# Kernel optimization log

Measured on AMD Instinct MI355X. Metric: run time of the kernel, lower is better.

Reference implementation:

```python
import jax, jax.numpy as jnp
import numpy as np

B, S, H, NH, HD = 2, 2048, 2048, 16, 128


def _bit_linear(x, w):
    """Ternary STE BitLinear: absmean scaling, round/clamp, fp matmul, rescale."""
    eps = 1e-5
    wn = w / (jnp.abs(w).mean() + eps)
    # straight-through estimator: forward uses quantized weights, grad flows to wn
    wq = wn + jax.lax.stop_gradient(jnp.clip(jnp.round(wn), -1.0, 1.0) - wn)
    y = x @ wq.T
    scale = w.shape[1]  # in_features
    Qb = 128.0  # 2**(8-1)
    return jnp.clip(y / scale * Qb, -Qb, Qb)


def _rotate_half(x):
    x1, x2 = jnp.split(x, 2, axis=-1)
    return jnp.concatenate([-x2, x1], axis=-1)


def setup_inputs() -> dict:
    key = jax.random.key(0)
    k1, k2, k3 = jax.random.split(key, 3)
    x = jax.random.normal(k1, (B, S, H), dtype=jnp.float32)
    w_qkv = jax.random.normal(k2, (3 * H, H), dtype=jnp.float32) * 0.02
    w_o = jax.random.normal(k3, (H, H), dtype=jnp.float32) * 0.02
    # realistic RoPE table [2, S, HD]
    inv_freq = 1.0 / (10000.0 ** (jnp.arange(0, HD, 2, dtype=jnp.float32) / HD))
    freqs = jnp.arange(S, dtype=jnp.float32)[:, None] * inv_freq[None, :]
    emb = jnp.concatenate([freqs, freqs], axis=-1)  # [S, HD]
    rotary = jnp.stack([jnp.cos(emb), jnp.sin(emb)], axis=0)
    return {"x": x, "rotary": rotary, "w_qkv": w_qkv, "w_o": w_o}


def reference(x, rotary, w_qkv, w_o):
    qkv = _bit_linear(x, w_qkv)  # [B, S, 3H]
    q, k, v = jnp.split(qkv, 3, axis=-1)
    q = q.reshape(B, S, NH, HD)
    k = k.reshape(B, S, NH, HD)
    v = v.reshape(B, S, NH, HD)
    cos = rotary[0][None, :, None, :]  # [1, S, 1, HD]
    sin = rotary[1][None, :, None, :]
    q = q * cos + _rotate_half(q) * sin
    k = k * cos + _rotate_half(k) * sin
    # [B, NH, S, HD]
    q, k, v = (t.transpose(0, 2, 1, 3) for t in (q, k, v))
    scores = jnp.einsum("bhqd,bhkd->bhqk", q, k) / np.sqrt(HD).astype(np.float32)
    causal = jnp.tril(jnp.ones((S, S), dtype=bool))
    scores = jnp.where(causal[None, None], scores, -jnp.inf)
    attn = jax.nn.softmax(scores, axis=-1)
    y = jnp.einsum("bhqk,bhkd->bhqd", attn, v)
    y = y.transpose(0, 2, 1, 3).reshape(B, S, H)
    return _bit_linear(y, w_o)
```

## Files before the change

### kernel.cpp

```cpp
#include <hip/hip_runtime.h>
#include <hip/hip_bf16.h>
#include <stdint.h>

#define B_   2
#define S_   2048
#define H_   2048
#define NH_  16
#define HD_  128
#define MTOK 4096
#define NQKV 6144

typedef unsigned short u16;
typedef __attribute__((ext_vector_type(8))) __bf16 bf16x8;
typedef __attribute__((ext_vector_type(4))) float f32x4;
typedef __attribute__((ext_vector_type(16))) float f32x16;

static __device__ __forceinline__ float bf2f(u16 u){
  union { uint32_t i; float f; } v; v.i = ((uint32_t)u) << 16; return v.f;
}
static __device__ __forceinline__ u16 f2bf(float f){
  union { float f; uint32_t i; } v; v.f = f;
  uint32_t r = v.i + 0x7FFFu + ((v.i >> 16) & 1u);
  return (u16)(r >> 16);
}
static __device__ __forceinline__ uint32_t cvt_pk_bf16(float lo, float hi){
  uint32_t r;
  asm("v_cvt_pk_bf16_f32 %0, %1, %2" : "=v"(r) : "v"(lo), "v"(hi));
  return r;
}
static __device__ __forceinline__ void pl32swap(uint32_t &a, uint32_t &b){
  asm volatile("v_permlane32_swap_b32 %0, %1" : "+v"(a), "+v"(b));
}

__device__ __forceinline__ void gload_lds16(const void* g, void* l){
  __builtin_amdgcn_global_load_lds((const __attribute__((address_space(1))) void*)g,
                                   (__attribute__((address_space(3))) void*)l, 16, 0, 0);
}

__global__ void absum_kernel(const float* __restrict__ w, int n, float* __restrict__ partial){
  __shared__ float sm[256];
  float s = 0.f;
  for (int i = blockIdx.x*256 + threadIdx.x; i < n; i += gridDim.x*256)
    s += fabsf(w[i]);
  sm[threadIdx.x] = s; __syncthreads();
  for (int st = 128; st > 0; st >>= 1){
    if ((int)threadIdx.x < st) sm[threadIdx.x] += sm[threadIdx.x + st];
    __syncthreads();
  }
  if (threadIdx.x == 0) partial[blockIdx.x] = sm[0];
}

__global__ void finalize_kernel(const float* __restrict__ p1, const float* __restrict__ p2,
                                float* __restrict__ scales){
  __shared__ double sm[256];
  int t = threadIdx.x;
  double s = (double)p1[t] + (double)p1[t+256] + (double)p1[t+512] + (double)p1[t+768];
  sm[t] = s; __syncthreads();
  for (int st = 128; st > 0; st >>= 1){ if (t < st) sm[t] += sm[t+st]; __syncthreads(); }
  if (t == 0) scales[0] = (float)(1.0 / (sm[0] / (double)(3*H_*H_) + 1e-5));
  __syncthreads();
  s = (double)p2[t] + (double)p2[t+256] + (double)p2[t+512] + (double)p2[t+768];
  sm[t] = s; __syncthreads();
  for (int st = 128; st > 0; st >>= 1){ if (t < st) sm[t] += sm[t+st]; __syncthreads(); }
  if (t == 0) scales[1] = (float)(1.0 / (sm[0] / (double)(H_*H_) + 1e-5));
}

__global__ void quant_kernel(const float* __restrict__ w, u16* __restrict__ wq, int n,
                             const float* __restrict__ scales, int which){
  float inv = scales[which];
  for (int i = blockIdx.x*256 + threadIdx.x; i < n; i += gridDim.x*256){
    float q = rintf(w[i] * inv);
    q = fminf(1.f, fmaxf(-1.f, q));
    wq[i] = f2bf(q);
  }
}

__global__ void castx_kernel(const float* __restrict__ x, u16* __restrict__ xb, int n){
  int i = blockIdx.x*256 + threadIdx.x;
  if (i < n) xb[i] = f2bf(x[i]);
}

template<int EPI>
__global__ __launch_bounds__(256, 4) void gemm_kernel(const u16* __restrict__ A,
    const u16* __restrict__ Bw, int M, int N, int K,
    float* __restrict__ outf, u16* __restrict__ qb, u16* __restrict__ kb, u16* __restrict__ vtb)
{
  __shared__ u16 As[128*32];
  __shared__ u16 Bs[128*32];
  int nbn = N >> 7;
  int nb_tot = (M >> 7) * nbn;
  int bid = blockIdx.x;
  int chunk = nb_tot >> 3;
  bid = (bid & 7) * chunk + (bid >> 3);
  int bm = bid / nbn, bn = bid % nbn;
  int m0 = bm << 7, n0 = bn << 7;
  int tid = threadIdx.x;
  int lane = tid & 63, wid = tid >> 6;
  int wr = wid >> 1, wc = wid & 1;
  int lg = lane >> 4, lr = lane & 15;

  const u16* Ab = A + m0 * K;
  const u16* Bb = Bw + n0 * K;
  int srow = tid >> 2;
  int scol = (tid & 3) << 3;

  f32x4 acc[4][4];
  #pragma unroll
  for (int i = 0; i < 4; i++)
    #pragma unroll
    for (int j = 0; j < 4; j++) acc[i][j] = f32x4{0.f,0.f,0.f,0.f};

  for (int k0 = 0; k0 < K; k0 += 32){
    gload_lds16(Ab + srow*K      + k0 + scol, As + tid*8);
    gload_lds16(Ab + (srow+64)*K + k0 + scol, As + 2048 + tid*8);
    gload_lds16(Bb + srow*K      + k0 + scol, Bs + tid*8);
    gload_lds16(Bb + (srow+64)*K + k0 + scol, Bs + 2048 + tid*8);
    __syncthreads();
    bf16x8 af[4], bfr[4];
    #pragma unroll
    for (int mi = 0; mi < 4; mi++) af[mi]  = *(const bf16x8*)(As + ((wr*64 + mi*16 + lr)*32 + lg*8));
    #pragma unroll
    for (int ni = 0; ni < 4; ni++) bfr[ni] = *(const bf16x8*)(Bs + ((wc*64 + ni*16 + lr)*32 + lg*8));
    #pragma unroll
    for (int mi = 0; mi < 4; mi++)
      #pragma unroll
      for (int ni = 0; ni < 4; ni++)
        acc[mi][ni] = __builtin_amdgcn_mfma_f32_16x16x32_bf16(af[mi], bfr[ni], acc[mi][ni], 0, 0, 0);
    __syncthreads();
  }

  #pragma unroll
  for (int mi = 0; mi < 4; mi++){
    #pragma unroll
    for (int ni = 0; ni < 4; ni++){
      int ncol = n0 + wc*64 + ni*16 + lr;
      #pragma unroll
      for (int r = 0; r < 4; r++){
        int m = m0 + wr*64 + mi*16 + lg*4 + r;
        float v = acc[mi][ni][r] * 0.0625f;
        v = fminf(128.f, fmaxf(-128.f, v));
        if (EPI == 1){
          outf[m*N + ncol] = v;
        } else {
          int b = m >> 11, s = m & 2047;
          int part = ncol >> 11, c = ncol & 2047;
          int h = c >> 7, d = c & 127;
          int bh = b*NH_ + h;
          u16 bv = f2bf(v);
          if (part == 0)      qb[((bh*S_ + s) << 7) + d] = bv;
          else if (part == 1) kb[((bh*S_ + s) << 7) + d] = bv;
          else                vtb[((bh*HD_ + d) << 11) + s] = bv;
        }
      }
    }
  }
}

__global__ void rope_kernel(u16* __restrict__ qb, u16* __restrict__ kb, const float* __restrict__ rot){
  int i = blockIdx.x*256 + threadIdx.x;
  int d = i & 63;
  int s = (i >> 6) & 2047;
  int bh = (i >> 17) & 31;
  u16* buf = (i >> 22) ? kb : qb;
  int base = (bh*S_ + s)*HD_;
  float c  = rot[s*HD_ + d];
  float sn = rot[S_*HD_ + s*HD_ + d];
  float x1 = bf2f(buf[base + d]);
  float x2 = bf2f(buf[base + d + 64]);
  buf[base + d]      = f2bf(x1*c - x2*sn);
  buf[base + d + 64] = f2bf(x2*c + x1*sn);
}

__global__ __launch_bounds__(256) void attn_kernel(const u16* __restrict__ qb,
    const u16* __restrict__ kb, const u16* __restrict__ vtb, u16* __restrict__ ao)
{
  __shared__ alignas(16) u16 Ks[2][4096];
  __shared__ alignas(16) u16 Vs[2][4096];

  int bid = blockIdx.x;
  int sbid = (bid & 7)*64 + (bid >> 3);
  int bh = sbid >> 4;
  int bq = 15 - (sbid & 15);
  int tid = threadIdx.x;
  int wid = tid >> 6, lane = tid & 63;
  int l31 = lane & 31, hl = lane >> 5;
  int q0 = bq * 128;
  int qw = q0 + wid*32;
  int q  = qw + l31;

  const u16* Qp = qb + (size_t)(bh*S_ + qw)*HD_;
  const u16* Kp = kb + (size_t)bh*S_*HD_;
  const u16* Vt = vtb + (size_t)bh*HD_*S_;

  bf16x8 qf[8];
  #pragma unroll
  for (int t = 0; t < 8; t++)
    qf[t] = *(const bf16x8*)(Qp + l31*HD_ + t*16 + hl*8);

  f32x16 o[4];
  #pragma unroll
  for (int i = 0; i < 4; i++)
    #pragma unroll
    for (int j = 0; j < 16; j++) o[i][j] = 0.f;
  float m_r = -1e30f, l_r = 0.f;
  const float sm_scale = 0.08838834764831845f;

  auto STAGE = [&](int buf, int kt2){
    int t0 = wid*2;
    gload_lds16(Kp + (size_t)(kt2 + l31)*HD_ + (t0  )*16 + hl*8, &Ks[buf][((t0  )*64 + lane)*8]);
    gload_lds16(Kp + (size_t)(kt2 + l31)*HD_ + (t0+1)*16 + hl*8, &Ks[buf][((t0+1)*64 + lane)*8]);
    int v0 = wid*2, v1 = wid*2 + 1;
    gload_lds16(Vt + (size_t)((v0&3)*32 + l31)*S_ + kt2 + (v0>>2)*16 + hl*8, &Vs[buf][(v0*64 + lane)*8]);
    gload_lds16(Vt + (size_t)((v1&3)*32 + l31)*S_ + kt2 + (v1>>2)*16 + hl*8, &Vs[buf][(v1*64 + lane)*8]);
  };

  int n_it = 4*bq + 4;
  STAGE(0, 0);
  int cur = 0, kt = 0;
  for (int it = 0; it < n_it; ++it, kt += 32){
    if (it + 1 < n_it){
      STAGE(cur ^ 1, kt + 32);
      asm volatile("s_waitcnt vmcnt(4)" ::: "memory");
    } else {
      asm volatile("s_waitcnt vmcnt(0)" ::: "memory");
    }
    __builtin_amdgcn_sched_barrier(0);
    __builtin_amdgcn_s_barrier();

    if (kt <= qw){
      f32x16 sa;
      #pragma unroll
      for (int j = 0; j < 16; j++) sa[j] = 0.f;
      #pragma unroll
      for (int t = 0; t < 8; t++){
        bf16x8 kf = *(const bf16x8*)(&Ks[cur][(t*64 + lane)*8]);
        sa = __builtin_amdgcn_mfma_f32_32x32x16_bf16(kf, qf[t], sa, 0, 0, 0);
      }

      float sv[16];
      if (kt == qw){
        #pragma unroll
        for (int r = 0; r < 16; r++){
          int key = kt + (r&3) + 8*(r>>2) + 4*hl;
          sv[r] = (key > q) ? -1e30f : sa[r]*sm_scale;
        }
      } else {
        #pragma unroll
        for (int r = 0; r < 16; r++) sv[r] = sa[r]*sm_scale;
      }

      float pm = sv[0];
      #pragma unroll
      for (int r = 1; r < 16; r++) pm = fmaxf(pm, sv[r]);
      pm = fmaxf(pm, __shfl_xor(pm, 32));
      if (!__all(pm - m_r <= 8.f)){
        float mn = fmaxf(m_r, pm);
        float scl = __expf(m_r - mn);
        m_r = mn; l_r *= scl;
        #pragma unroll
        for (int i = 0; i < 4; i++)
          #pragma unroll
          for (int j = 0; j < 16; j++) o[i][j] *= scl;
      }
      float p[16];
      #pragma unroll
      for (int r = 0; r < 16; r++) p[r] = __expf(sv[r] - m_r);
      float ts = 0.f;
      #pragma unroll
      for (int r = 0; r < 16; r++) ts += p[r];
      ts += __shfl_xor(ts, 32);
      l_r += ts;

      uint32_t a0 = cvt_pk_bf16(p[0],  p[1]),  a1 = cvt_pk_bf16(p[2],  p[3]);
      uint32_t a2 = cvt_pk_bf16(p[4],  p[5]),  a3 = cvt_pk_bf16(p[6],  p[7]);
      uint32_t b0 = cvt_pk_bf16(p[8],  p[9]),  b1 = cvt_pk_bf16(p[10], p[11]);
      uint32_t b2 = cvt_pk_bf16(p[12], p[13]), b3 = cvt_pk_bf16(p[14], p[15]);
      pl32swap(a0, a2); pl32swap(a1, a3);
      pl32swap(b0, b2); pl32swap(b1, b3);
      union { uint32_t u[4]; bf16x8 v; } pf0, pf1;
      pf0.u[0]=a0; pf0.u[1]=a1; pf0.u[2]=a2; pf0.u[3]=a3;
      pf1.u[0]=b0; pf1.u[1]=b1; pf1.u[2]=b2; pf1.u[3]=b3;

      #pragma unroll
      for (int db = 0; db < 4; db++){
        bf16x8 vf0 = *(const bf16x8*)(&Vs[cur][((0*4 + db)*64 + lane)*8]);
        o[db] = __builtin_amdgcn_mfma_f32_32x32x16_bf16(vf0, pf0.v, o[db], 0, 0, 0);
        bf16x8 vf1 = *(const bf16x8*)(&Vs[cur][((1*4 + db)*64 + lane)*8]);
        o[db] = __builtin_amdgcn_mfma_f32_32x32x16_bf16(vf1, pf1.v, o[db], 0, 0, 0);
      }
      asm volatile("s_waitcnt lgkmcnt(0)" ::: "memory");
    }
    __builtin_amdgcn_sched_barrier(0);
    __builtin_amdgcn_s_barrier();
    cur ^= 1;
  }

  float inv = 1.f / l_r;
  int b = bh >> 4, hh = bh & 15;
  u16* orow = ao + (size_t)(b*S_ + q)*H_ + hh*HD_;
  #pragma unroll
  for (int db = 0; db < 4; db++){
    #pragma unroll
    for (int g = 0; g < 4; g++){
      ushort4 pk4;
      pk4.x = f2bf(o[db][4*g+0]*inv);
      pk4.y = f2bf(o[db][4*g+1]*inv);
      pk4.z = f2bf(o[db][4*g+2]*inv);
      pk4.w = f2bf(o[db][4*g+3]*inv);
      *(ushort4*)(orow + db*32 + g*8 + hl*4) = pk4;
    }
  }
}

extern "C" void kernel_launch(void* const* d_in, const int* in_sizes, int n_in,
                              void* d_out, int out_size, void* d_ws, size_t ws_size,
                              hipStream_t stream) {
  const float* x      = (const float*)d_in[0];
  const float* rotary = (const float*)d_in[1];
  const float* w_qkv  = (const float*)d_in[2];
  const float* w_o    = (const float*)d_in[3];
  float* out = (float*)d_out;

  char* wsb = (char*)d_ws;
  float* part_qkv = (float*)wsb;
  float* part_o   = part_qkv + 1024;
  float* scales   = part_o + 1024;
  size_t off = 16384;
  u16* xb    = (u16*)(wsb + off); off += (size_t)MTOK*H_*2;
  u16* wqkvq = (u16*)(wsb + off); off += (size_t)NQKV*H_*2;
  u16* woq   = (u16*)(wsb + off); off += (size_t)H_*H_*2;
  u16* qbuf  = (u16*)(wsb + off); off += (size_t)B_*NH_*S_*HD_*2;
  u16* kbuf  = (u16*)(wsb + off); off += (size_t)B_*NH_*S_*HD_*2;
  u16* vtb   = (u16*)(wsb + off); off += (size_t)B_*NH_*S_*HD_*2;
  u16* ao    = (u16*)(wsb + off); off += (size_t)MTOK*H_*2;

  absum_kernel<<<1024, 256, 0, stream>>>(w_qkv, 3*H_*H_, part_qkv);
  absum_kernel<<<1024, 256, 0, stream>>>(w_o, H_*H_, part_o);
  finalize_kernel<<<1, 256, 0, stream>>>(part_qkv, part_o, scales);
  quant_kernel<<<4096, 256, 0, stream>>>(w_qkv, wqkvq, 3*H_*H_, scales, 0);
  quant_kernel<<<2048, 256, 0, stream>>>(w_o, woq, H_*H_, scales, 1);
  castx_kernel<<<(MTOK*H_)/256, 256, 0, stream>>>(x, xb, MTOK*H_);

  gemm_kernel<0><<<(MTOK/128)*(NQKV/128), 256, 0, stream>>>(xb, wqkvq, MTOK, NQKV, H_,
                                                            nullptr, qbuf, kbuf, vtb);
  rope_kernel<<<(2*B_*NH_*S_*64)/256, 256, 0, stream>>>(qbuf, kbuf, rotary);
  attn_kernel<<<B_*NH_*(S_/128), 256, 0, stream>>>(qbuf, kbuf, vtb, ao);
  gemm_kernel<1><<<(MTOK/128)*(H_/128), 256, 0, stream>>>(ao, woq, MTOK, H_, H_,
                                                          out, nullptr, nullptr, nullptr);
}
```

Measured before the change: 381.4 us.

## Fuse quant/cast kernels and widen QKV GEMM tile to 128x256

Merges the two weight-quantization launches and the activation cast into one grid-stride kernel, removing two launches. Splits the templated GEMM into a dedicated QKV kernel with 512 threads and a 128x256 output tile, so each A tile loaded into LDS is reused across twice as many columns. The output-projection GEMM keeps the original 128x128 tiling. The wider tile uses more LDS per block and the 512-thread launch bound may limit occupancy, and the fused elementwise kernel adds per-element branching.

```diff
diff --git a/kernel.cpp b/kernel.cpp
--- a/kernel.cpp
+++ b/kernel.cpp
@@ -65,26 +65,101 @@
   if (t == 0) scales[1] = (float)(1.0 / (sm[0] / (double)(H_*H_) + 1e-5));
 }
 
-__global__ void quant_kernel(const float* __restrict__ w, u16* __restrict__ wq, int n,
-                             const float* __restrict__ scales, int which){
-  float inv = scales[which];
-  for (int i = blockIdx.x*256 + threadIdx.x; i < n; i += gridDim.x*256){
-    float q = rintf(w[i] * inv);
-    q = fminf(1.f, fmaxf(-1.f, q));
-    wq[i] = f2bf(q);
-  }
-}
-
-__global__ void castx_kernel(const float* __restrict__ x, u16* __restrict__ xb, int n){
-  int i = blockIdx.x*256 + threadIdx.x;
-  if (i < n) xb[i] = f2bf(x[i]);
-}
-
-template<int EPI>
-__global__ __launch_bounds__(256, 4) void gemm_kernel(const u16* __restrict__ A,
-    const u16* __restrict__ Bw, int M, int N, int K,
-    float* __restrict__ outf, u16* __restrict__ qb, u16* __restrict__ kb, u16* __restrict__ vtb)
+__global__ void quantcast_kernel(const float* __restrict__ w_qkv, const float* __restrict__ w_o,
+                                 const float* __restrict__ x, u16* __restrict__ wqkvq,
+                                 u16* __restrict__ woq, u16* __restrict__ xb,
+                                 const float* __restrict__ scales){
+  const int n1 = 3*H_*H_, n2 = H_*H_, n3 = MTOK*H_;
+  float inv0 = scales[0], inv1 = scales[1];
+  for (int i = blockIdx.x*256 + threadIdx.x; i < n1 + n2 + n3; i += gridDim.x*256){
+    if (i < n1){
+      float q = rintf(w_qkv[i] * inv0);
+      wqkvq[i] = f2bf(fminf(1.f, fmaxf(-1.f, q)));
+    } else if (i < n1 + n2){
+      int j = i - n1;
+      float q = rintf(w_o[j] * inv1);
+      woq[j] = f2bf(fminf(1.f, fmaxf(-1.f, q)));
+    } else {
+      int j = i - n1 - n2;
+      xb[j] = f2bf(x[j]);
+    }
+  }
+}
+
+__global__ __launch_bounds__(512, 4) void gemmqkv_kernel(const u16* __restrict__ A,
+    const u16* __restrict__ Bw, u16* __restrict__ qb, u16* __restrict__ kb, u16* __restrict__ vtb)
 {
+  const int M = MTOK, N = NQKV, K = H_;
+  __shared__ u16 As[128*32];
+  __shared__ u16 Bs[256*32];
+  int nbn = N >> 8;
+  int nb_tot = (M >> 7) * nbn;
+  int bid = blockIdx.x;
+  int chunk = nb_tot >> 3;
+  bid = (bid & 7) * chunk + (bid >> 3);
+  int bm = bid / nbn, bn = bid % nbn;
+  int m0 = bm << 7, n0 = bn << 8;
+  int tid = threadIdx.x;
+  int lane = tid & 63, wid = tid >> 6;
+  int wr = wid >> 2, wc = wid & 3;
+  int lg = lane >> 4, lr = lane & 15;
+
+  const u16* Ab = A + (size_t)m0 * K;
+  const u16* Bb = Bw + (size_t)n0 * K;
+  int srow = tid >> 2;
+  int scol = (tid & 3) << 3;
+
+  f32x4 acc[4][4];
+  #pragma unroll
+  for (int i = 0; i < 4; i++)
+    #pragma unroll
+    for (int j = 0; j < 4; j++) acc[i][j] = f32x4{0.f,0.f,0.f,0.f};
+
+  for (int k0 = 0; k0 < K; k0 += 32){
+    gload_lds16(Ab + (size_t)srow*K        + k0 + scol, As + tid*8);
+    gload_lds16(Bb + (size_t)srow*K        + k0 + scol, Bs + tid*8);
+    gload_lds16(Bb + (size_t)(srow+128)*K  + k0 + scol, Bs + 4096 + tid*8);
+    __syncthreads();
+    bf16x8 af[4], bfr[4];
+    #pragma unroll
+    for (int mi = 0; mi < 4; mi++) af[mi]  = *(const bf16x8*)(As + ((wr*64 + mi*16 + lr)*32 + lg*8));
+    #pragma unroll
+    for (int ni = 0; ni < 4; ni++) bfr[ni] = *(const bf16x8*)(Bs + ((wc*64 + ni*16 + lr)*32 + lg*8));
+    #pragma unroll
+    for (int mi = 0; mi < 4; mi++)
+      #pragma unroll
+      for (int ni = 0; ni < 4; ni++)
+        acc[mi][ni] = __builtin_amdgcn_mfma_f32_16x16x32_bf16(af[mi], bfr[ni], acc[mi][ni], 0, 0, 0);
+    __syncthreads();
+  }
+
+  #pragma unroll
+  for (int mi = 0; mi < 4; mi++){
+    #pragma unroll
+    for (int ni = 0; ni < 4; ni++){
+      int ncol = n0 + wc*64 + ni*16 + lr;
+      #pragma unroll
+      for (int r = 0; r < 4; r++){
+        int m = m0 + wr*64 + mi*16 + lg*4 + r;
+        float v = acc[mi][ni][r] * 0.0625f;
+        v = fminf(128.f, fmaxf(-128.f, v));
+        int b = m >> 11, s = m & 2047;
+        int part = ncol >> 11, c = ncol & 2047;
+        int h = c >> 7, d = c & 127;
+        int bh = b*NH_ + h;
+        u16 bv = f2bf(v);
+        if (part == 0)      qb[((bh*S_ + s) << 7) + d] = bv;
+        else if (part == 1) kb[((bh*S_ + s) << 7) + d] = bv;
+        else                vtb[((bh*HD_ + d) << 11) + s] = bv;
+      }
+    }
+  }
+}
+
+__global__ __launch_bounds__(256, 4) void gemmo_kernel(const u16* __restrict__ A,
+    const u16* __restrict__ Bw, float* __restrict__ outf)
+{
+  const int M = MTOK, N = H_, K = H_;
   __shared__ u16 As[128*32];
   __shared__ u16 Bs[128*32];
   int nbn = N >> 7;
@@ -139,18 +214,7 @@
         int m = m0 + wr*64 + mi*16 + lg*4 + r;
         float v = acc[mi][ni][r] * 0.0625f;
         v = fminf(128.f, fmaxf(-128.f, v));
-        if (EPI == 1){
-          outf[m*N + ncol] = v;
-        } else {
-          int b = m >> 11, s = m & 2047;
-          int part = ncol >> 11, c = ncol & 2047;
-          int h = c >> 7, d = c & 127;
-          int bh = b*NH_ + h;
-          u16 bv = f2bf(v);
-          if (part == 0)      qb[((bh*S_ + s) << 7) + d] = bv;
-          else if (part == 1) kb[((bh*S_ + s) << 7) + d] = bv;
-          else                vtb[((bh*HD_ + d) << 11) + s] = bv;
-        }
+        outf[(size_t)m*N + ncol] = v;
       }
     }
   }
@@ -337,14 +401,10 @@
   absum_kernel<<<1024, 256, 0, stream>>>(w_qkv, 3*H_*H_, part_qkv);
   absum_kernel<<<1024, 256, 0, stream>>>(w_o, H_*H_, part_o);
   finalize_kernel<<<1, 256, 0, stream>>>(part_qkv, part_o, scales);
-  quant_kernel<<<4096, 256, 0, stream>>>(w_qkv, wqkvq, 3*H_*H_, scales, 0);
-  quant_kernel<<<2048, 256, 0, stream>>>(w_o, woq, H_*H_, scales, 1);
-  castx_kernel<<<(MTOK*H_)/256, 256, 0, stream>>>(x, xb, MTOK*H_);
-
-  gemm_kernel<0><<<(MTOK/128)*(NQKV/128), 256, 0, stream>>>(xb, wqkvq, MTOK, NQKV, H_,
-                                                            nullptr, qbuf, kbuf, vtb);
+  quantcast_kernel<<<2048, 256, 0, stream>>>(w_qkv, w_o, x, wqkvq, woq, xb, scales);
+
+  gemmqkv_kernel<<<(MTOK/128)*(NQKV/256), 512, 0, stream>>>(xb, wqkvq, qbuf, kbuf, vtb);
   rope_kernel<<<(2*B_*NH_*S_*64)/256, 256, 0, stream>>>(qbuf, kbuf, rotary);
   attn_kernel<<<B_*NH_*(S_/128), 256, 0, stream>>>(qbuf, kbuf, vtb, ao);
-  gemm_kernel<1><<<(MTOK/128)*(H_/128), 256, 0, stream>>>(ao, woq, MTOK, H_, H_,
-                                                          out, nullptr, nullptr, nullptr);
-}
+  gemmo_kernel<<<(MTOK/128)*(H_/128), 256, 0, stream>>>(ao, woq, out);
+}
```

Measured after the change: 382.8 us (median of 2 runs). Within noise of the previous version (+0.4%).
